# Performance work log

Measured on AMD Instinct MI355X. Metric: run time of the kernel, lower is better.

Reference implementation:

```python
import jax, jax.numpy as jnp
import numpy as np

N_T, D_MODEL, RANK, BATCH = 64, 1024, 8, 4096
THRESHOLD = 0.0  # jumprelu threshold (forward default)


def setup_inputs() -> dict:
    key = jax.random.key(0)
    k_x, k_v, k_u, k_e = jax.random.split(key, 4)
    scale = (1.0 / (D_MODEL * RANK)) ** 0.25
    x = jax.random.normal(k_x, (BATCH, D_MODEL), dtype=jnp.float32)
    V = jax.random.normal(k_v, (N_T, RANK, D_MODEL), dtype=jnp.float32) * scale
    U = jax.random.normal(k_u, (N_T, D_MODEL, RANK), dtype=jnp.float32) * scale
    encoder = jax.random.normal(k_e, (N_T, D_MODEL), dtype=jnp.float32)
    encoder = encoder / jnp.linalg.norm(encoder, axis=1, keepdims=True)
    bias = -jnp.ones((N_T,), dtype=jnp.float32)  # init_constant(bias, -1.0)
    return {"x": x, "V": V, "U": U, "encoder": encoder, "bias": bias}


def jumprelu(x, threshold=THRESHOLD):
    # forward: hard threshold x * 1[x > threshold]
    return x * (x > threshold).astype(x.dtype)


def reference(x, V, U, encoder, bias):
    # pre_acts: (batch, n)
    pre_acts = x @ encoder.T - bias
    gate = jumprelu(pre_acts)  # activation_fn='jumprelu', threshold=0.0
    # Vx: (n, batch, rank)
    Vx = jnp.einsum('nrd,bd->nbr', V, x)
    # UVx: (n, batch, d) -- the large intermediate a fused kernel would avoid
    UVx = jnp.einsum('ndr,nbr->nbd', U, Vx)
    # gated sum over transforms: (batch, d)
    output = jnp.einsum('nbd,bn->bd', UVx, gate)
    u_norms = jnp.linalg.norm(U.reshape(U.shape[0], -1), axis=1)
    v_norms = jnp.linalg.norm(V.reshape(V.shape[0], -1), axis=1)
    frobenius_norms = u_norms * v_norms / (D_MODEL * RANK) ** 0.5
    return output, gate, frobenius_norms
```

## Files before the change

kernel.cpp:

```cpp
#include <hip/hip_runtime.h>
#include <math.h>

#define BATCHN 4096
#define DMODEL 1024
#define NT 64
#define RANK 8
#define K2 512

typedef __attribute__((ext_vector_type(8))) short bf16x8;
typedef __attribute__((ext_vector_type(4))) float f32x4;

__device__ __forceinline__ void async16(void* lds, const void* g) {
    __builtin_amdgcn_global_load_lds(
        (const __attribute__((address_space(1))) void*)g,
        (__attribute__((address_space(3))) void*)lds, 16, 0, 0);
}

__device__ __forceinline__ short f2bf(float f) {
    unsigned u = __builtin_bit_cast(unsigned, f);
    u += 0x7fffu + ((u >> 16) & 1u);
    return (short)(u >> 16);
}

__global__ __launch_bounds__(256) void convert_kernel(
    const float* __restrict__ x, const float* __restrict__ enc,
    const float* __restrict__ V, const float* __restrict__ U,
    unsigned short* __restrict__ xb, unsigned short* __restrict__ Wb,
    unsigned short* __restrict__ Ub,
    float* __restrict__ su_part, float* __restrict__ sv_part)
{
    const int b = blockIdx.x, t = threadIdx.x;
    const float* src;
    unsigned short* dst;
    float* psum = nullptr;
    if (b < 2048) {
        const int e0 = b * 2048 + t * 8;
        src = x + e0; dst = xb + e0;
    } else if (b < 2336) {
        const int e0 = (b - 2048) * 2048 + t * 8;
        const int row = e0 >> 10, col = e0 & 1023;
        if (row < 64) {
            src = enc + (size_t)row * 1024 + col;
        } else {
            src = V + (size_t)(row - 64) * 1024 + col;
            const int vrow = (b - 2048) * 2 - 64;
            psum = sv_part + (vrow >> 3) * 4 + ((vrow & 7) >> 1);
        }
        dst = Wb + e0;
    } else {
        const int bi = b - 2336;
        const int e0 = bi * 2048 + t * 8;
        src = U + e0; dst = Ub + e0;
        psum = su_part + (bi >> 2) * 4 + (bi & 3);
    }
    float4 v0 = *(const float4*)src;
    float4 v1 = *(const float4*)(src + 4);
    bf16x8 o;
    o[0] = f2bf(v0.x); o[1] = f2bf(v0.y); o[2] = f2bf(v0.z); o[3] = f2bf(v0.w);
    o[4] = f2bf(v1.x); o[5] = f2bf(v1.y); o[6] = f2bf(v1.z); o[7] = f2bf(v1.w);
    *(bf16x8*)dst = o;

    if (psum) {
        float s = v0.x*v0.x + v0.y*v0.y + v0.z*v0.z + v0.w*v0.w
                + v1.x*v1.x + v1.y*v1.y + v1.z*v1.z + v1.w*v1.w;
        #pragma unroll
        for (int off = 32; off; off >>= 1) s += __shfl_down(s, off);
        __shared__ float red[4];
        if ((t & 63) == 0) red[t >> 6] = s;
        __syncthreads();
        if (t == 0) *psum = red[0] + red[1] + red[2] + red[3];
    }
}

__global__ __launch_bounds__(256) void gatevx_kernel(
    const unsigned short* __restrict__ A, const unsigned short* __restrict__ Bm,
    const float* __restrict__ bias,
    float* __restrict__ gate_out, unsigned short* __restrict__ vx_out)
{
    constexpr int BK = 64, KDIM = DMODEL;
    __shared__ unsigned short As[64 * BK];
    __shared__ unsigned short Bs[64 * BK];
    const int t = threadIdx.x;
    const int wave = t >> 6, lane = t & 63;
    const int bm = blockIdx.y, bn = blockIdx.x;
    const int wm = wave & 1, wn = wave >> 1;
    const int lrow = lane >> 3, lchunk = lane & 7;
    const int l15 = lane & 15, lq = lane >> 4;

    f32x4 acc[2][2] = {};
    const size_t Abase = (size_t)bm * 64 * KDIM;
    const size_t Bbase = (size_t)bn * 64 * KDIM;

    for (int k0 = 0; k0 < KDIM; k0 += BK) {
        #pragma unroll
        for (int c = 0; c < 2; ++c) {
            const int row = (wave * 2 + c) * 8 + lrow;
            const int chunk = lchunk ^ lrow;
            async16(&As[(wave * 2 + c) * 512],
                    A + Abase + (size_t)row * KDIM + k0 + chunk * 8);
            async16(&Bs[(wave * 2 + c) * 512],
                    Bm + Bbase + (size_t)row * KDIM + k0 + chunk * 8);
        }
        __syncthreads();
        #pragma unroll
        for (int s = 0; s < 2; ++s) {
            bf16x8 af[2], bfr[2];
            const int kc = s * 4 + lq;
            #pragma unroll
            for (int i = 0; i < 2; ++i) {
                const int m = wm * 32 + i * 16 + l15;
                af[i] = *(const bf16x8*)&As[m * BK + ((kc ^ (m & 7)) * 8)];
            }
            #pragma unroll
            for (int j = 0; j < 2; ++j) {
                const int n = wn * 32 + j * 16 + l15;
                bfr[j] = *(const bf16x8*)&Bs[n * BK + ((kc ^ (n & 7)) * 8)];
            }
            #pragma unroll
            for (int i = 0; i < 2; ++i)
                #pragma unroll
                for (int j = 0; j < 2; ++j)
                    acc[i][j] = __builtin_amdgcn_mfma_f32_16x16x32_bf16(
                        af[i], bfr[j], acc[i][j], 0, 0, 0);
        }
        __syncthreads();
    }

    #pragma unroll
    for (int i = 0; i < 2; ++i) {
        const int rowb = bm * 64 + wm * 32 + i * 16 + lq * 4;
        #pragma unroll
        for (int j = 0; j < 2; ++j) {
            const int col = wn * 32 + j * 16 + l15;
            #pragma unroll
            for (int r = 0; r < 4; ++r) {
                const int row = rowb + r;
                const float v = acc[i][j][r];
                if (bn == 0) {
                    const float p = v - bias[col];
                    gate_out[(size_t)row * NT + col] = p > 0.f ? p : 0.f;
                } else {
                    vx_out[(size_t)row * K2 + (bn - 1) * 64 + col] = (unsigned short)f2bf(v);
                }
            }
        }
    }
}

__global__ __launch_bounds__(256) void out_kernel(
    const unsigned short* __restrict__ vx, const float* __restrict__ gate,
    const unsigned short* __restrict__ Ub, float* __restrict__ out,
    const float* __restrict__ su_part, const float* __restrict__ sv_part,
    float* __restrict__ fro)
{
    constexpr int BK = 64, KDIM = K2;
    __shared__ unsigned short As[64 * BK];
    __shared__ unsigned short Bs[8 * 2 * 64 * 8];
    const int t = threadIdx.x;
    const int wave = t >> 6, lane = t & 63;
    const int bm = blockIdx.y, bn = blockIdx.x;
    const int wm = wave & 1, wn = wave >> 1;
    const int lrow = lane >> 3, lchunk = lane & 7;
    const int l15 = lane & 15, lq = lane >> 4;

    f32x4 acc[2][4] = {};

    for (int k0 = 0; k0 < KDIM; k0 += BK) {
        #pragma unroll
        for (int c = 0; c < 2; ++c) {
            const int row = (wave * 2 + c) * 8 + lrow;
            const int grow = bm * 64 + row;
            const int chunk = lchunk ^ lrow;
            bf16x8 v = *(const bf16x8*)(vx + (size_t)grow * K2 + k0 + chunk * 8);
            const float g = gate[(size_t)grow * NT + (k0 >> 3) + chunk];
            bf16x8 o;
            #pragma unroll
            for (int e = 0; e < 8; ++e) {
                const float f = __builtin_bit_cast(float,
                    ((unsigned)(unsigned short)v[e]) << 16);
                o[e] = (short)(__builtin_bit_cast(unsigned, f * g) >> 16);
            }
            *(bf16x8*)&As[(wave * 2 + c) * 512 + lane * 8] = o;
        }
        #pragma unroll
        for (int c = 0; c < 4; ++c) {
            const int n_local = wave * 2 + (c >> 1);
            const int dblk = c & 1;
            const int n_glob = (k0 >> 3) + n_local;
            async16(&Bs[(n_local * 2 + dblk) * 512],
                    Ub + (size_t)n_glob * (DMODEL * RANK)
                       + (size_t)(bn * 128 + dblk * 64 + lane) * RANK);
        }
        __syncthreads();
        #pragma unroll
        for (int s = 0; s < 2; ++s) {
            bf16x8 af[2], bfr[4];
            const int kc = s * 4 + lq;
            #pragma unroll
            for (int i = 0; i < 2; ++i) {
                const int m = wm * 32 + i * 16 + l15;
                af[i] = *(const bf16x8*)&As[m * BK + ((kc ^ (m & 7)) * 8)];
            }
            #pragma unroll
            for (int j = 0; j < 4; ++j) {
                const int cl = wn * 64 + j * 16 + l15;
                bfr[j] = *(const bf16x8*)&Bs[((kc * 2 + (cl >> 6)) * 64 + (cl & 63)) * 8];
            }
            #pragma unroll
            for (int i = 0; i < 2; ++i)
                #pragma unroll
                for (int j = 0; j < 4; ++j)
                    acc[i][j] = __builtin_amdgcn_mfma_f32_16x16x32_bf16(
                        af[i], bfr[j], acc[i][j], 0, 0, 0);
        }
        __syncthreads();
    }

    #pragma unroll
    for (int i = 0; i < 2; ++i) {
        const int rowb = bm * 64 + wm * 32 + i * 16 + lq * 4;
        #pragma unroll
        for (int j = 0; j < 4; ++j) {
            const int col = bn * 128 + wn * 64 + j * 16 + l15;
            #pragma unroll
            for (int r = 0; r < 4; ++r)
                out[(size_t)(rowb + r) * DMODEL + col] = acc[i][j][r];
        }
    }

    if (bn == 0 && bm == 0 && t < NT) {
        float su = su_part[t * 4] + su_part[t * 4 + 1] + su_part[t * 4 + 2] + su_part[t * 4 + 3];
        float sv = sv_part[t * 4] + sv_part[t * 4 + 1] + sv_part[t * 4 + 2] + sv_part[t * 4 + 3];
        fro[t] = sqrtf(su) * sqrtf(sv) / sqrtf((float)(DMODEL * RANK));
    }
}

extern "C" void kernel_launch(void* const* d_in, const int* in_sizes, int n_in,
                              void* d_out, int out_size, void* d_ws, size_t ws_size,
                              hipStream_t stream) {
    const float* x    = (const float*)d_in[0];
    const float* V    = (const float*)d_in[1];
    const float* U    = (const float*)d_in[2];
    const float* enc  = (const float*)d_in[3];
    const float* bias = (const float*)d_in[4];

    float* out  = (float*)d_out;
    float* gate = out + (size_t)BATCHN * DMODEL;
    float* fro  = gate + (size_t)BATCHN * NT;

    char* ws = (char*)d_ws;
    unsigned short* xb = (unsigned short*)ws;
    unsigned short* Wb = (unsigned short*)(ws + 8388608);
    unsigned short* Ub = (unsigned short*)(ws + 9568256);
    unsigned short* vx = (unsigned short*)(ws + 10616832);
    float* su_part     = (float*)(ws + 14811136);
    float* sv_part     = (float*)(ws + 14812160);

    convert_kernel<<<2592, 256, 0, stream>>>(x, enc, V, U, xb, Wb, Ub, su_part, sv_part);
    gatevx_kernel<<<dim3(9, 64), 256, 0, stream>>>(xb, Wb, bias, gate, vx);
    out_kernel<<<dim3(8, 64), 256, 0, stream>>>(vx, gate, Ub, out, su_part, sv_part, fro);
}
```

Before: 106.0 us.

## Double-buffer LDS tiles in gate/Vx and output GEMM kernels

Both GEMM kernels now keep two LDS buffers. The next K-tile is loaded into one buffer (async global-to-LDS for B, register prefetch for the gated A tile) while MFMAs run on the other. Each iteration then needs one barrier instead of two. The aim is to hide global load latency behind compute, at the cost of doubled LDS use, which may lower occupancy, and extra registers for the prefetched A values.

Result: slower. 109.8 us (+3.6%).

```diff
diff --git a/kernel.cpp b/kernel.cpp
--- a/kernel.cpp
+++ b/kernel.cpp
@@ -77,9 +77,9 @@
     const float* __restrict__ bias,
     float* __restrict__ gate_out, unsigned short* __restrict__ vx_out)
 {
-    constexpr int BK = 64, KDIM = DMODEL;
-    __shared__ unsigned short As[64 * BK];
-    __shared__ unsigned short Bs[64 * BK];
+    constexpr int BK = 64, KDIM = DMODEL, NIT = KDIM / BK;
+    __shared__ unsigned short As[2][64 * BK];
+    __shared__ unsigned short Bs[2][64 * BK];
     const int t = threadIdx.x;
     const int wave = t >> 6, lane = t & 63;
     const int bm = blockIdx.y, bn = blockIdx.x;
@@ -91,17 +91,18 @@
     const size_t Abase = (size_t)bm * 64 * KDIM;
     const size_t Bbase = (size_t)bn * 64 * KDIM;
 
-    for (int k0 = 0; k0 < KDIM; k0 += BK) {
+    auto STAGE = [&](int buf, int k0) {
         #pragma unroll
         for (int c = 0; c < 2; ++c) {
             const int row = (wave * 2 + c) * 8 + lrow;
             const int chunk = lchunk ^ lrow;
-            async16(&As[(wave * 2 + c) * 512],
+            async16(&As[buf][(wave * 2 + c) * 512],
                     A + Abase + (size_t)row * KDIM + k0 + chunk * 8);
-            async16(&Bs[(wave * 2 + c) * 512],
+            async16(&Bs[buf][(wave * 2 + c) * 512],
                     Bm + Bbase + (size_t)row * KDIM + k0 + chunk * 8);
         }
-        __syncthreads();
+    };
+    auto COMPUTE = [&](int buf) {
         #pragma unroll
         for (int s = 0; s < 2; ++s) {
             bf16x8 af[2], bfr[2];
@@ -109,12 +110,12 @@
             #pragma unroll
             for (int i = 0; i < 2; ++i) {
                 const int m = wm * 32 + i * 16 + l15;
-                af[i] = *(const bf16x8*)&As[m * BK + ((kc ^ (m & 7)) * 8)];
+                af[i] = *(const bf16x8*)&As[buf][m * BK + ((kc ^ (m & 7)) * 8)];
             }
             #pragma unroll
             for (int j = 0; j < 2; ++j) {
                 const int n = wn * 32 + j * 16 + l15;
-                bfr[j] = *(const bf16x8*)&Bs[n * BK + ((kc ^ (n & 7)) * 8)];
+                bfr[j] = *(const bf16x8*)&Bs[buf][n * BK + ((kc ^ (n & 7)) * 8)];
             }
             #pragma unroll
             for (int i = 0; i < 2; ++i)
@@ -123,8 +124,18 @@
                     acc[i][j] = __builtin_amdgcn_mfma_f32_16x16x32_bf16(
                         af[i], bfr[j], acc[i][j], 0, 0, 0);
         }
+    };
+
+    STAGE(0, 0);
+    __syncthreads();
+    int cur = 0;
+    for (int kt = 0; kt < NIT - 1; ++kt) {
+        STAGE(cur ^ 1, (kt + 1) * BK);
+        COMPUTE(cur);
         __syncthreads();
-    }
+        cur ^= 1;
+    }
+    COMPUTE(cur);
 
     #pragma unroll
     for (int i = 0; i < 2; ++i) {
@@ -153,9 +164,9 @@
     const float* __restrict__ su_part, const float* __restrict__ sv_part,
     float* __restrict__ fro)
 {
-    constexpr int BK = 64, KDIM = K2;
-    __shared__ unsigned short As[64 * BK];
-    __shared__ unsigned short Bs[8 * 2 * 64 * 8];
+    constexpr int BK = 64, KDIM = K2, NIT = KDIM / BK;
+    __shared__ unsigned short As[2][64 * BK];
+    __shared__ unsigned short Bs[2][8 * 2 * 64 * 8];
     const int t = threadIdx.x;
     const int wave = t >> 6, lane = t & 63;
     const int bm = blockIdx.y, bn = blockIdx.x;
@@ -165,33 +176,41 @@
 
     f32x4 acc[2][4] = {};
 
-    for (int k0 = 0; k0 < KDIM; k0 += BK) {
+    auto LOADA = [&](int k0, bf16x8* v, float* g) {
         #pragma unroll
         for (int c = 0; c < 2; ++c) {
             const int row = (wave * 2 + c) * 8 + lrow;
             const int grow = bm * 64 + row;
             const int chunk = lchunk ^ lrow;
-            bf16x8 v = *(const bf16x8*)(vx + (size_t)grow * K2 + k0 + chunk * 8);
-            const float g = gate[(size_t)grow * NT + (k0 >> 3) + chunk];
+            v[c] = *(const bf16x8*)(vx + (size_t)grow * K2 + k0 + chunk * 8);
+            g[c] = gate[(size_t)grow * NT + (k0 >> 3) + chunk];
+        }
+    };
+    auto WRITEA = [&](int buf, const bf16x8* v, const float* g) {
+        #pragma unroll
+        for (int c = 0; c < 2; ++c) {
             bf16x8 o;
             #pragma unroll
             for (int e = 0; e < 8; ++e) {
                 const float f = __builtin_bit_cast(float,
-                    ((unsigned)(unsigned short)v[e]) << 16);
-                o[e] = (short)(__builtin_bit_cast(unsigned, f * g) >> 16);
-            }
-            *(bf16x8*)&As[(wave * 2 + c) * 512 + lane * 8] = o;
-        }
+                    ((unsigned)(unsigned short)v[c][e]) << 16);
+                o[e] = (short)(__builtin_bit_cast(unsigned, f * g[c]) >> 16);
+            }
+            *(bf16x8*)&As[buf][(wave * 2 + c) * 512 + lane * 8] = o;
+        }
+    };
+    auto STAGEB = [&](int buf, int k0) {
         #pragma unroll
         for (int c = 0; c < 4; ++c) {
             const int n_local = wave * 2 + (c >> 1);
             const int dblk = c & 1;
             const int n_glob = (k0 >> 3) + n_local;
-            async16(&Bs[(n_local * 2 + dblk) * 512],
+            async16(&Bs[buf][(n_local * 2 + dblk) * 512],
                     Ub + (size_t)n_glob * (DMODEL * RANK)
                        + (size_t)(bn * 128 + dblk * 64 + lane) * RANK);
         }
-        __syncthreads();
+    };
+    auto COMPUTE = [&](int buf) {
         #pragma unroll
         for (int s = 0; s < 2; ++s) {
             bf16x8 af[2], bfr[4];
@@ -199,12 +218,12 @@
             #pragma unroll
             for (int i = 0; i < 2; ++i) {
                 const int m = wm * 32 + i * 16 + l15;
-                af[i] = *(const bf16x8*)&As[m * BK + ((kc ^ (m & 7)) * 8)];
+                af[i] = *(const bf16x8*)&As[buf][m * BK + ((kc ^ (m & 7)) * 8)];
             }
             #pragma unroll
             for (int j = 0; j < 4; ++j) {
                 const int cl = wn * 64 + j * 16 + l15;
-                bfr[j] = *(const bf16x8*)&Bs[((kc * 2 + (cl >> 6)) * 64 + (cl & 63)) * 8];
+                bfr[j] = *(const bf16x8*)&Bs[buf][((kc * 2 + (cl >> 6)) * 64 + (cl & 63)) * 8];
             }
             #pragma unroll
             for (int i = 0; i < 2; ++i)
@@ -213,8 +232,26 @@
                     acc[i][j] = __builtin_amdgcn_mfma_f32_16x16x32_bf16(
                         af[i], bfr[j], acc[i][j], 0, 0, 0);
         }
+    };
+
+    {
+        bf16x8 v[2]; float g[2];
+        LOADA(0, v, g);
+        STAGEB(0, 0);
+        WRITEA(0, v, g);
+    }
+    __syncthreads();
+    int cur = 0;
+    for (int kt = 0; kt < NIT - 1; ++kt) {
+        bf16x8 v[2]; float g[2];
+        LOADA((kt + 1) * BK, v, g);
+        STAGEB(cur ^ 1, (kt + 1) * BK);
+        COMPUTE(cur);
+        WRITEA(cur ^ 1, v, g);
         __syncthreads();
-    }
+        cur ^= 1;
+    }
+    COMPUTE(cur);
 
     #pragma unroll
     for (int i = 0; i < 2; ++i) {
```
